# Kernel tuning notes

Hardware: AMD Instinct MI355X
Metric: run time of the kernel (lower is better)

The kernel has to match this reference:

```python
import jax, jax.numpy as jnp
import numpy as np
from jax import lax

T, IN, H, B = 256, 2048, 2048, 8
K_INIT = 4.0

def setup_inputs() -> dict:
    key = jax.random.key(0)
    k1, k2, k3, k4, k5, k6 = jax.random.split(key, 6)
    k = 1.0 / np.sqrt(H)
    # simplex-init alphas: off-diagonal -K, diagonal log(1-(B-1)exp(-K)), plus small noise
    base = jnp.full((B, B), -K_INIT) + jnp.eye(B) * (np.log(1.0 - (B - 1) * np.exp(-K_INIT)) + K_INIT)
    alphas = base + 0.01 * jax.random.normal(k1, (B, B))
    return {
        "x": jax.random.normal(k2, (T, IN), dtype=jnp.float32),            # sentence of word vectors
        "W": jax.random.uniform(k3, (B, H, H), minval=-k, maxval=k),       # B recurrent basis matrices
        "alphas": alphas.astype(jnp.float32),                               # [B, B] mixing logits
        "bias": jax.random.uniform(k4, (H,), minval=-k, maxval=k),
        "v": jnp.eye(H, IN, dtype=jnp.float32),                             # input projection (init = eye)
        "fc_w": jax.random.uniform(k5, (H, H), minval=-k, maxval=k),
        "fc_b": jax.random.uniform(k6, (H,), minval=-k, maxval=k),
        "alpha_int": 0,
    }

def reference(x, W, alphas, bias, v, fc_w, fc_b, alpha_int):
    # normalise_alpha == softmax over the selected alpha row (simplex=True)
    alpha = jax.nn.softmax(alphas[alpha_int])                 # [B]
    u = jnp.einsum('b,bij->ij', alpha, W)                     # mixed recurrent weight [H, H]
    igates = x @ v.T                                          # all input gates at once [T, H]

    def step(h, ig):                                          # Elman cell: h = tanh(v@w + u@h + bias)
        h = jnp.tanh(ig + u @ h + bias)
        return h, None

    h0 = jnp.zeros((H,), dtype=x.dtype)
    h, _ = lax.scan(step, h0, igates)                         # sequential over T words
    out = jax.nn.sigmoid(h @ fc_w.T + fc_b)                   # fc(hidden.t()) then sigmoid
    return out[None, :]                                       # [1, H]
```

## Files before the change

kernel.cpp:

```cpp
#include <hip/hip_runtime.h>
#include <math.h>

#define HDIM    2048
#define TSTEPS  256
#define BBASIS  8

typedef float f32x4 __attribute__((ext_vector_type(4)));

__device__ inline void store_coherent_f4(float* p, f32x4 v) {
    asm volatile("global_store_dwordx4 %0, %1, off sc0 sc1"
                 :: "v"(p), "v"(v) : "memory");
}
__device__ inline f32x4 load_coherent_f4(const float* p) {
    f32x4 a;
    asm volatile("global_load_dwordx4 %0, %1, off sc0 sc1\n\t"
                 "s_waitcnt vmcnt(0)"
                 : "=&v"(a) : "v"(p) : "memory");
    return a;
}

__global__ __launch_bounds__(256, 1)
void prep_kernel(const float* __restrict__ x,
                 const float* __restrict__ W,
                 const float* __restrict__ alphas,
                 const float* __restrict__ v,
                 const int*   __restrict__ alpha_int,
                 float*       __restrict__ u_g,
                 float*       __restrict__ ig_g)
{
    const int tid  = threadIdx.x;
    const int bid  = blockIdx.x;
    const int wave = tid >> 6;
    const int lane = tid & 63;
    const int r0   = bid * 8 + wave * 2;

    __shared__ __align__(16) float x_tile[8][HDIM];

    const int ai = alpha_int[0];
    float a[BBASIS];
    float mx = -1e30f;
    #pragma unroll
    for (int b = 0; b < BBASIS; ++b) { a[b] = alphas[ai * BBASIS + b]; mx = fmaxf(mx, a[b]); }
    float ssum = 0.f;
    #pragma unroll
    for (int b = 0; b < BBASIS; ++b) { a[b] = expf(a[b] - mx); ssum += a[b]; }
    const float inv_s = 1.f / ssum;

    {
        float acc[2][8][4];
        #pragma unroll
        for (int q = 0; q < 2; ++q)
            #pragma unroll
            for (int k = 0; k < 8; ++k)
                #pragma unroll
                for (int i = 0; i < 4; ++i) acc[q][k][i] = 0.f;

        for (int b = 0; b < BBASIS; ++b) {
            const float ab = a[b] * inv_s;
            #pragma unroll
            for (int q = 0; q < 2; ++q) {
                const f32x4* wrow = (const f32x4*)(W + ((size_t)b * HDIM + (size_t)(r0 + q)) * HDIM);
                #pragma unroll
                for (int k = 0; k < 8; ++k) {
                    f32x4 w4 = wrow[lane + 64 * k];
                    acc[q][k][0] += ab * w4.x;
                    acc[q][k][1] += ab * w4.y;
                    acc[q][k][2] += ab * w4.z;
                    acc[q][k][3] += ab * w4.w;
                }
            }
        }
        #pragma unroll
        for (int q = 0; q < 2; ++q) {
            f32x4* urow = (f32x4*)(u_g + (size_t)(r0 + q) * HDIM);
            #pragma unroll
            for (int k = 0; k < 8; ++k) {
                f32x4 w4;
                w4.x = acc[q][k][0]; w4.y = acc[q][k][1];
                w4.z = acc[q][k][2]; w4.w = acc[q][k][3];
                urow[lane + 64 * k] = w4;
            }
        }
    }

    {
        float vr[2][8][4];
        #pragma unroll
        for (int q = 0; q < 2; ++q) {
            const f32x4* vrow = (const f32x4*)(v + (size_t)(r0 + q) * HDIM);
            #pragma unroll
            for (int k = 0; k < 8; ++k) {
                f32x4 t4 = vrow[lane + 64 * k];
                vr[q][k][0] = t4.x; vr[q][k][1] = t4.y; vr[q][k][2] = t4.z; vr[q][k][3] = t4.w;
            }
        }
        for (int tb = 0; tb < TSTEPS; tb += 8) {
            #pragma unroll
            for (int j = 0; j < 8; ++j) {
                const f32x4* xt4 = (const f32x4*)(x + (size_t)(tb + j) * HDIM);
                #pragma unroll
                for (int c = 0; c < 2; ++c)
                    ((f32x4*)x_tile[j])[tid + 256 * c] = xt4[tid + 256 * c];
            }
            __syncthreads();
            #pragma unroll
            for (int j = 0; j < 8; ++j) {
                float acc0 = 0.f, acc1 = 0.f;
                #pragma unroll
                for (int k = 0; k < 8; ++k) {
                    const f32x4 x4 = ((const f32x4*)x_tile[j])[lane + 64 * k];
                    acc0 += vr[0][k][0]*x4.x + vr[0][k][1]*x4.y + vr[0][k][2]*x4.z + vr[0][k][3]*x4.w;
                    acc1 += vr[1][k][0]*x4.x + vr[1][k][1]*x4.y + vr[1][k][2]*x4.z + vr[1][k][3]*x4.w;
                }
                #pragma unroll
                for (int off = 32; off > 0; off >>= 1) {
                    acc0 += __shfl_xor(acc0, off, 64);
                    acc1 += __shfl_xor(acc1, off, 64);
                }
                if (lane == 0)
                    *(float2*)&ig_g[(size_t)(tb + j) * HDIM + r0] = make_float2(acc0, acc1);
            }
            __syncthreads();
        }
    }
}

__global__ __launch_bounds__(512, 1)
void scan_kernel(const float* __restrict__ bias,
                 const float* __restrict__ fc_w,
                 const float* __restrict__ fc_b,
                 float*       __restrict__ out,
                 const float* __restrict__ u_g,
                 const float* __restrict__ ig_g,
                 float*       __restrict__ hbuf)
{
    const int tid  = threadIdx.x;
    const int bid  = blockIdx.x;
    const int wave = tid >> 6;
    const int lane = tid & 63;
    const int r0   = bid * 32 + wave * 4;

    __shared__ __align__(16) float h_lds[2][HDIM];
    __shared__ __align__(16) float ig_lds[TSTEPS][32];

    #pragma unroll
    for (int i = 0; i < 4; ++i) {
        const int c  = tid + 512 * i;
        const int t  = c >> 3;
        const int ch = c & 7;
        f32x4 g = *(const f32x4*)&ig_g[(size_t)t * HDIM + bid * 32 + ch * 4];
        *(f32x4*)&ig_lds[t][ch * 4] = g;
    }

    float u_reg[4][8][4];
    #pragma unroll
    for (int q = 0; q < 4; ++q) {
        const f32x4* urow = (const f32x4*)(u_g + (size_t)(r0 + q) * HDIM);
        #pragma unroll
        for (int k = 0; k < 8; ++k) {
            f32x4 w4 = urow[lane + 64 * k];
            u_reg[q][k][0] = w4.x; u_reg[q][k][1] = w4.y;
            u_reg[q][k][2] = w4.z; u_reg[q][k][3] = w4.w;
        }
    }
    float bias4[4];
    #pragma unroll
    for (int q = 0; q < 4; ++q) bias4[q] = bias[r0 + q];

    h_lds[0][tid]        = 0.f;
    h_lds[0][tid + 512]  = 0.f;
    h_lds[0][tid + 1024] = 0.f;
    h_lds[0][tid + 1536] = 0.f;
    __syncthreads();

    int cur = 0;
    for (int t = 0; t < TSTEPS; ++t) {
        float acc0 = 0.f, acc1 = 0.f, acc2 = 0.f, acc3 = 0.f;
        #pragma unroll
        for (int k = 0; k < 8; ++k) {
            const f32x4 h4 = ((const f32x4*)h_lds[cur])[lane + 64 * k];
            acc0 += u_reg[0][k][0]*h4.x + u_reg[0][k][1]*h4.y + u_reg[0][k][2]*h4.z + u_reg[0][k][3]*h4.w;
            acc1 += u_reg[1][k][0]*h4.x + u_reg[1][k][1]*h4.y + u_reg[1][k][2]*h4.z + u_reg[1][k][3]*h4.w;
            acc2 += u_reg[2][k][0]*h4.x + u_reg[2][k][1]*h4.y + u_reg[2][k][2]*h4.z + u_reg[2][k][3]*h4.w;
            acc3 += u_reg[3][k][0]*h4.x + u_reg[3][k][1]*h4.y + u_reg[3][k][2]*h4.z + u_reg[3][k][3]*h4.w;
        }
        #pragma unroll
        for (int off = 32; off > 0; off >>= 1) {
            acc0 += __shfl_xor(acc0, off, 64);
            acc1 += __shfl_xor(acc1, off, 64);
            acc2 += __shfl_xor(acc2, off, 64);
            acc3 += __shfl_xor(acc3, off, 64);
        }
        float* hg = hbuf + (size_t)(t + 1) * HDIM;
        if (lane == 0) {
            const f32x4 ig4 = *(const f32x4*)&ig_lds[t][wave * 4];
            f32x4 hv;
            hv.x = tanhf(acc0 + ig4.x + bias4[0]);
            hv.y = tanhf(acc1 + ig4.y + bias4[1]);
            hv.z = tanhf(acc2 + ig4.z + bias4[2]);
            hv.w = tanhf(acc3 + ig4.w + bias4[3]);
            store_coherent_f4(hg + r0, hv);
        }
        const float* pp = hg + 4 * tid;
        f32x4 hq = load_coherent_f4(pp);
        const unsigned s = 0xFFFFFFFFu;
        while ((__float_as_uint(hq.x) == s) | (__float_as_uint(hq.y) == s) |
               (__float_as_uint(hq.z) == s) | (__float_as_uint(hq.w) == s)) {
            __builtin_amdgcn_s_sleep(1);
            hq = load_coherent_f4(pp);
        }
        const int nxt = cur ^ 1;
        *(f32x4*)&h_lds[nxt][4 * tid] = hq;
        __syncthreads();
        cur = nxt;
    }

    {
        float acc0 = 0.f, acc1 = 0.f, acc2 = 0.f, acc3 = 0.f;
        const f32x4* f0 = (const f32x4*)(fc_w + (size_t)(r0 + 0) * HDIM);
        const f32x4* f1 = (const f32x4*)(fc_w + (size_t)(r0 + 1) * HDIM);
        const f32x4* f2 = (const f32x4*)(fc_w + (size_t)(r0 + 2) * HDIM);
        const f32x4* f3 = (const f32x4*)(fc_w + (size_t)(r0 + 3) * HDIM);
        #pragma unroll
        for (int k = 0; k < 8; ++k) {
            const f32x4 h4 = ((const f32x4*)h_lds[cur])[lane + 64 * k];
            f32x4 w0 = f0[lane + 64 * k];
            f32x4 w1 = f1[lane + 64 * k];
            f32x4 w2 = f2[lane + 64 * k];
            f32x4 w3 = f3[lane + 64 * k];
            acc0 += w0.x*h4.x + w0.y*h4.y + w0.z*h4.z + w0.w*h4.w;
            acc1 += w1.x*h4.x + w1.y*h4.y + w1.z*h4.z + w1.w*h4.w;
            acc2 += w2.x*h4.x + w2.y*h4.y + w2.z*h4.z + w2.w*h4.w;
            acc3 += w3.x*h4.x + w3.y*h4.y + w3.z*h4.z + w3.w*h4.w;
        }
        #pragma unroll
        for (int off = 32; off > 0; off >>= 1) {
            acc0 += __shfl_xor(acc0, off, 64);
            acc1 += __shfl_xor(acc1, off, 64);
            acc2 += __shfl_xor(acc2, off, 64);
            acc3 += __shfl_xor(acc3, off, 64);
        }
        if (lane == 0) {
            f32x4 o4;
            o4.x = 1.f / (1.f + expf(-(acc0 + fc_b[r0 + 0])));
            o4.y = 1.f / (1.f + expf(-(acc1 + fc_b[r0 + 1])));
            o4.z = 1.f / (1.f + expf(-(acc2 + fc_b[r0 + 2])));
            o4.w = 1.f / (1.f + expf(-(acc3 + fc_b[r0 + 3])));
            *(f32x4*)&out[r0] = o4;
        }
    }
}

__global__ __launch_bounds__(512, 1)
void elman_scan_self(const float* __restrict__ x,
                     const float* __restrict__ W,
                     const float* __restrict__ alphas,
                     const float* __restrict__ bias,
                     const float* __restrict__ v,
                     const float* __restrict__ fc_w,
                     const float* __restrict__ fc_b,
                     const int*   __restrict__ alpha_int,
                     float*       __restrict__ out,
                     float*       __restrict__ hbuf)
{
    const int tid  = threadIdx.x;
    const int bid  = blockIdx.x;
    const int wave = tid >> 6;
    const int lane = tid & 63;
    const int r0   = bid * 32 + wave * 4;

    __shared__ __align__(16) float x_tile[8][HDIM];
    __shared__ __align__(16) float ig_lds[TSTEPS][32];
    __shared__ __align__(16) float h_lds[2][HDIM];

    const int ai = alpha_int[0];
    float a[BBASIS];
    float mx = -1e30f;
    #pragma unroll
    for (int b = 0; b < BBASIS; ++b) { a[b] = alphas[ai * BBASIS + b]; mx = fmaxf(mx, a[b]); }
    float ssum = 0.f;
    #pragma unroll
    for (int b = 0; b < BBASIS; ++b) { a[b] = expf(a[b] - mx); ssum += a[b]; }
    const float inv_s = 1.f / ssum;

    {
        float vr[4][8][4];
        #pragma unroll
        for (int q = 0; q < 4; ++q) {
            const f32x4* vrow = (const f32x4*)(v + (size_t)(r0 + q) * HDIM);
            #pragma unroll
            for (int k = 0; k < 8; ++k) {
                f32x4 t4 = vrow[lane + 64 * k];
                vr[q][k][0] = t4.x; vr[q][k][1] = t4.y; vr[q][k][2] = t4.z; vr[q][k][3] = t4.w;
            }
        }
        for (int tb = 0; tb < TSTEPS; tb += 8) {
            #pragma unroll
            for (int j = 0; j < 8; ++j)
                *(f32x4*)&x_tile[j][4 * tid] =
                    *(const f32x4*)&x[(size_t)(tb + j) * HDIM + 4 * tid];
            __syncthreads();
            #pragma unroll
            for (int j = 0; j < 8; ++j) {
                float acc0 = 0.f, acc1 = 0.f, acc2 = 0.f, acc3 = 0.f;
                #pragma unroll
                for (int k = 0; k < 8; ++k) {
                    const f32x4 x4 = ((const f32x4*)x_tile[j])[lane + 64 * k];
                    acc0 += vr[0][k][0]*x4.x + vr[0][k][1]*x4.y + vr[0][k][2]*x4.z + vr[0][k][3]*x4.w;
                    acc1 += vr[1][k][0]*x4.x + vr[1][k][1]*x4.y + vr[1][k][2]*x4.z + vr[1][k][3]*x4.w;
                    acc2 += vr[2][k][0]*x4.x + vr[2][k][1]*x4.y + vr[2][k][2]*x4.z + vr[2][k][3]*x4.w;
                    acc3 += vr[3][k][0]*x4.x + vr[3][k][1]*x4.y + vr[3][k][2]*x4.z + vr[3][k][3]*x4.w;
                }
                #pragma unroll
                for (int off = 32; off > 0; off >>= 1) {
                    acc0 += __shfl_xor(acc0, off, 64);
                    acc1 += __shfl_xor(acc1, off, 64);
                    acc2 += __shfl_xor(acc2, off, 64);
                    acc3 += __shfl_xor(acc3, off, 64);
                }
                if (lane == 0) {
                    f32x4 ig4; ig4.x = acc0; ig4.y = acc1; ig4.z = acc2; ig4.w = acc3;
                    *(f32x4*)&ig_lds[tb + j][wave * 4] = ig4;
                }
            }
            __syncthreads();
        }
    }

    float u_reg[4][8][4];
    #pragma unroll
    for (int q = 0; q < 4; ++q)
        #pragma unroll
        for (int k = 0; k < 8; ++k)
            #pragma unroll
            for (int i = 0; i < 4; ++i) u_reg[q][k][i] = 0.f;

    for (int b = 0; b < BBASIS; ++b) {
        const float ab = a[b] * inv_s;
        #pragma unroll
        for (int q = 0; q < 4; ++q) {
            const f32x4* wrow = (const f32x4*)(W + ((size_t)b * HDIM + (size_t)(r0 + q)) * HDIM);
            #pragma unroll
            for (int k = 0; k < 8; ++k) {
                f32x4 w4 = wrow[lane + 64 * k];
                u_reg[q][k][0] += ab * w4.x;
                u_reg[q][k][1] += ab * w4.y;
                u_reg[q][k][2] += ab * w4.z;
                u_reg[q][k][3] += ab * w4.w;
            }
        }
    }
    float bias4[4];
    #pragma unroll
    for (int q = 0; q < 4; ++q) bias4[q] = bias[r0 + q];

    h_lds[0][tid] = 0.f; h_lds[0][tid + 512] = 0.f;
    h_lds[0][tid + 1024] = 0.f; h_lds[0][tid + 1536] = 0.f;
    __syncthreads();

    int cur = 0;
    for (int t = 0; t < TSTEPS; ++t) {
        float acc0 = 0.f, acc1 = 0.f, acc2 = 0.f, acc3 = 0.f;
        #pragma unroll
        for (int k = 0; k < 8; ++k) {
            const f32x4 h4 = ((const f32x4*)h_lds[cur])[lane + 64 * k];
            acc0 += u_reg[0][k][0]*h4.x + u_reg[0][k][1]*h4.y + u_reg[0][k][2]*h4.z + u_reg[0][k][3]*h4.w;
            acc1 += u_reg[1][k][0]*h4.x + u_reg[1][k][1]*h4.y + u_reg[1][k][2]*h4.z + u_reg[1][k][3]*h4.w;
            acc2 += u_reg[2][k][0]*h4.x + u_reg[2][k][1]*h4.y + u_reg[2][k][2]*h4.z + u_reg[2][k][3]*h4.w;
            acc3 += u_reg[3][k][0]*h4.x + u_reg[3][k][1]*h4.y + u_reg[3][k][2]*h4.z + u_reg[3][k][3]*h4.w;
        }
        #pragma unroll
        for (int off = 32; off > 0; off >>= 1) {
            acc0 += __shfl_xor(acc0, off, 64);
            acc1 += __shfl_xor(acc1, off, 64);
            acc2 += __shfl_xor(acc2, off, 64);
            acc3 += __shfl_xor(acc3, off, 64);
        }
        float* hg = hbuf + (size_t)(t + 1) * HDIM;
        if (lane == 0) {
            const f32x4 ig4 = *(const f32x4*)&ig_lds[t][wave * 4];
            f32x4 hv;
            hv.x = tanhf(acc0 + ig4.x + bias4[0]);
            hv.y = tanhf(acc1 + ig4.y + bias4[1]);
            hv.z = tanhf(acc2 + ig4.z + bias4[2]);
            hv.w = tanhf(acc3 + ig4.w + bias4[3]);
            store_coherent_f4(hg + r0, hv);
        }
        const float* pp = hg + 4 * tid;
        f32x4 hq = load_coherent_f4(pp);
        const unsigned s = 0xFFFFFFFFu;
        while ((__float_as_uint(hq.x) == s) | (__float_as_uint(hq.y) == s) |
               (__float_as_uint(hq.z) == s) | (__float_as_uint(hq.w) == s)) {
            __builtin_amdgcn_s_sleep(1);
            hq = load_coherent_f4(pp);
        }
        const int nxt = cur ^ 1;
        *(f32x4*)&h_lds[nxt][4 * tid] = hq;
        __syncthreads();
        cur = nxt;
    }

    {
        float acc0 = 0.f, acc1 = 0.f, acc2 = 0.f, acc3 = 0.f;
        const f32x4* f0 = (const f32x4*)(fc_w + (size_t)(r0 + 0) * HDIM);
        const f32x4* f1 = (const f32x4*)(fc_w + (size_t)(r0 + 1) * HDIM);
        const f32x4* f2 = (const f32x4*)(fc_w + (size_t)(r0 + 2) * HDIM);
        const f32x4* f3 = (const f32x4*)(fc_w + (size_t)(r0 + 3) * HDIM);
        #pragma unroll
        for (int k = 0; k < 8; ++k) {
            const f32x4 h4 = ((const f32x4*)h_lds[cur])[lane + 64 * k];
            f32x4 w0 = f0[lane + 64 * k];
            f32x4 w1 = f1[lane + 64 * k];
            f32x4 w2 = f2[lane + 64 * k];
            f32x4 w3 = f3[lane + 64 * k];
            acc0 += w0.x*h4.x + w0.y*h4.y + w0.z*h4.z + w0.w*h4.w;
            acc1 += w1.x*h4.x + w1.y*h4.y + w1.z*h4.z + w1.w*h4.w;
            acc2 += w2.x*h4.x + w2.y*h4.y + w2.z*h4.z + w2.w*h4.w;
            acc3 += w3.x*h4.x + w3.y*h4.y + w3.z*h4.z + w3.w*h4.w;
        }
        #pragma unroll
        for (int off = 32; off > 0; off >>= 1) {
            acc0 += __shfl_xor(acc0, off, 64);
            acc1 += __shfl_xor(acc1, off, 64);
            acc2 += __shfl_xor(acc2, off, 64);
            acc3 += __shfl_xor(acc3, off, 64);
        }
        if (lane == 0) {
            f32x4 o4;
            o4.x = 1.f / (1.f + expf(-(acc0 + fc_b[r0 + 0])));
            o4.y = 1.f / (1.f + expf(-(acc1 + fc_b[r0 + 1])));
            o4.z = 1.f / (1.f + expf(-(acc2 + fc_b[r0 + 2])));
            o4.w = 1.f / (1.f + expf(-(acc3 + fc_b[r0 + 3])));
            *(f32x4*)&out[r0] = o4;
        }
    }
}

extern "C" void kernel_launch(void* const* d_in, const int* in_sizes, int n_in,
                              void* d_out, int out_size, void* d_ws, size_t ws_size,
                              hipStream_t stream)
{
    const float* x      = (const float*)d_in[0];
    const float* W      = (const float*)d_in[1];
    const float* alphas = (const float*)d_in[2];
    const float* bias   = (const float*)d_in[3];
    const float* v      = (const float*)d_in[4];
    const float* fc_w   = (const float*)d_in[5];
    const float* fc_b   = (const float*)d_in[6];
    const int*   ai     = (const int*)d_in[7];
    float* out = (float*)d_out;

    const size_t HB_BYTES = (size_t)(TSTEPS + 1) * HDIM * sizeof(float);
    const size_t IG_OFF   = 0x210000;
    const size_t IG_BYTES = (size_t)TSTEPS * HDIM * sizeof(float);
    const size_t U_OFF    = IG_OFF + 0x210000;
    const size_t U_BYTES  = (size_t)HDIM * HDIM * sizeof(float);
    const size_t NEED     = U_OFF + U_BYTES;

    float* hbuf = (float*)d_ws;

    hipMemsetAsync(d_ws, 0xFF, HB_BYTES, stream);

    if (ws_size >= NEED) {
        float* ig_g = (float*)((char*)d_ws + IG_OFF);
        float* u_g  = (float*)((char*)d_ws + U_OFF);
        prep_kernel<<<256, 256, 0, stream>>>(x, W, alphas, v, ai, u_g, ig_g);
        scan_kernel<<<64, 512, 0, stream>>>(bias, fc_w, fc_b, out, u_g, ig_g, hbuf);
    } else {
        elman_scan_self<<<64, 512, 0, stream>>>(x, W, alphas, bias, v, fc_w, fc_b,
                                                ai, out, hbuf);
    }
}
```

Measured before the change: 1.033 ms.

## Replace full-history h buffer with replicated ring using value-offset phase flags

The per-step hidden-state exchange moves from a full T×H buffer with NaN sentinels to a small 4-slot ring. Each slot is replicated 8 times, so blocks poll different copies and spread contention across memory channels. Readiness is encoded by adding ±8 to tanh outputs, alternating every 4 steps, so no per-step reset is needed. The large memset also shrinks to a small zeroing of the ring. The risks are extra store traffic for the replicas and a small precision loss from the add/subtract of 8 on values in [-1,1].

```diff
diff --git a/kernel.cpp b/kernel.cpp
--- a/kernel.cpp
+++ b/kernel.cpp
@@ -4,6 +4,8 @@
 #define HDIM    2048
 #define TSTEPS  256
 #define BBASIS  8
+#define RING_D  4
+#define NR      8
 
 typedef float f32x4 __attribute__((ext_vector_type(4)));
 
@@ -132,7 +134,7 @@
                  float*       __restrict__ out,
                  const float* __restrict__ u_g,
                  const float* __restrict__ ig_g,
-                 float*       __restrict__ hbuf)
+                 float*       __restrict__ ring)
 {
     const int tid  = threadIdx.x;
     const int bid  = blockIdx.x;
@@ -191,24 +193,34 @@
             acc2 += __shfl_xor(acc2, off, 64);
             acc3 += __shfl_xor(acc3, off, 64);
         }
-        float* hg = hbuf + (size_t)(t + 1) * HDIM;
-        if (lane == 0) {
-            const f32x4 ig4 = *(const f32x4*)&ig_lds[t][wave * 4];
-            f32x4 hv;
-            hv.x = tanhf(acc0 + ig4.x + bias4[0]);
-            hv.y = tanhf(acc1 + ig4.y + bias4[1]);
-            hv.z = tanhf(acc2 + ig4.z + bias4[2]);
-            hv.w = tanhf(acc3 + ig4.w + bias4[3]);
-            store_coherent_f4(hg + r0, hv);
-        }
-        const float* pp = hg + 4 * tid;
+        const int   st     = t + 1;
+        const float bias_f = ((st >> 2) & 1) ? 8.0f : -8.0f;
+        float* slotbase = ring + (size_t)((st & (RING_D - 1)) * NR) * HDIM;
+
+        const f32x4 ig4 = *(const f32x4*)&ig_lds[t][wave * 4];
+        f32x4 hv;
+        hv.x = tanhf(acc0 + ig4.x + bias4[0]) + bias_f;
+        hv.y = tanhf(acc1 + ig4.y + bias4[1]) + bias_f;
+        hv.z = tanhf(acc2 + ig4.z + bias4[2]) + bias_f;
+        hv.w = tanhf(acc3 + ig4.w + bias4[3]) + bias_f;
+        if (lane < NR)
+            store_coherent_f4(slotbase + (size_t)lane * HDIM + r0, hv);
+
+        const float* pp = slotbase + (size_t)(bid & (NR - 1)) * HDIM + 4 * tid;
         f32x4 hq = load_coherent_f4(pp);
-        const unsigned s = 0xFFFFFFFFu;
-        while ((__float_as_uint(hq.x) == s) | (__float_as_uint(hq.y) == s) |
-               (__float_as_uint(hq.z) == s) | (__float_as_uint(hq.w) == s)) {
-            __builtin_amdgcn_s_sleep(1);
-            hq = load_coherent_f4(pp);
-        }
+        if (bias_f > 0.0f) {
+            while (!((hq.x > 6.5f) & (hq.y > 6.5f) & (hq.z > 6.5f) & (hq.w > 6.5f))) {
+                __builtin_amdgcn_s_sleep(1);
+                hq = load_coherent_f4(pp);
+            }
+        } else {
+            while (!((hq.x < -6.5f) & (hq.y < -6.5f) & (hq.z < -6.5f) & (hq.w < -6.5f))) {
+                __builtin_amdgcn_s_sleep(1);
+                hq = load_coherent_f4(pp);
+            }
+        }
+        hq.x -= bias_f; hq.y -= bias_f; hq.z -= bias_f; hq.w -= bias_f;
+
         const int nxt = cur ^ 1;
         *(f32x4*)&h_lds[nxt][4 * tid] = hq;
         __syncthreads();
@@ -450,23 +462,23 @@
     const int*   ai     = (const int*)d_in[7];
     float* out = (float*)d_out;
 
-    const size_t HB_BYTES = (size_t)(TSTEPS + 1) * HDIM * sizeof(float);
-    const size_t IG_OFF   = 0x210000;
-    const size_t IG_BYTES = (size_t)TSTEPS * HDIM * sizeof(float);
-    const size_t U_OFF    = IG_OFF + 0x210000;
-    const size_t U_BYTES  = (size_t)HDIM * HDIM * sizeof(float);
-    const size_t NEED     = U_OFF + U_BYTES;
-
-    float* hbuf = (float*)d_ws;
-
-    hipMemsetAsync(d_ws, 0xFF, HB_BYTES, stream);
+    const size_t RING_BYTES = (size_t)RING_D * NR * HDIM * sizeof(float);
+    const size_t IG_OFF     = 0x80000;
+    const size_t U_OFF      = IG_OFF + 0x200000;
+    const size_t U_BYTES    = (size_t)HDIM * HDIM * sizeof(float);
+    const size_t NEED       = U_OFF + U_BYTES;
 
     if (ws_size >= NEED) {
+        float* ring = (float*)d_ws;
         float* ig_g = (float*)((char*)d_ws + IG_OFF);
         float* u_g  = (float*)((char*)d_ws + U_OFF);
+        hipMemsetAsync(d_ws, 0, RING_BYTES, stream);
         prep_kernel<<<256, 256, 0, stream>>>(x, W, alphas, v, ai, u_g, ig_g);
-        scan_kernel<<<64, 512, 0, stream>>>(bias, fc_w, fc_b, out, u_g, ig_g, hbuf);
+        scan_kernel<<<64, 512, 0, stream>>>(bias, fc_w, fc_b, out, u_g, ig_g, (float*)ring);
     } else {
+        float* hbuf = (float*)d_ws;
+        const size_t hbuf_bytes = (size_t)(TSTEPS + 1) * HDIM * sizeof(float);
+        hipMemsetAsync(d_ws, 0xFF, hbuf_bytes, stream);
         elman_scan_self<<<64, 512, 0, stream>>>(x, W, alphas, bias, v, fc_w, fc_b,
                                                 ai, out, hbuf);
     }
```

New measurement: 995.5 us. 1.04x faster.
